# Kernel tuning notes

Measured on AMD Instinct MI355X. Metric: run time of the kernel, lower is better.

Reference implementation:

```python
import jax, jax.numpy as jnp
import numpy as np

N = 100000      # nodes
E = 1000000     # edges
H_DIM = 124     # node embedding dim
CLS_DIM = 4     # node class-logit dim (H_DIM + CLS_DIM = in_features = 128)
POLAR_DIM = 2   # edge_pred_features
HIDDEN = 256
OUT = 2
LN_EPS = 1e-5


def setup_inputs() -> dict:
    key = jax.random.key(0)
    ks = jax.random.split(key, 10)
    in_dim = 2 * (H_DIM + CLS_DIM) + POLAR_DIM  # 258
    return {
        "h": jax.random.normal(ks[0], (N, H_DIM), dtype=jnp.float32),
        "cls": jax.random.normal(ks[1], (N, CLS_DIM), dtype=jnp.float32),
        "polar": jax.random.normal(ks[2], (E, POLAR_DIM), dtype=jnp.float32),
        "src": jax.random.randint(ks[3], (E,), 0, N, dtype=jnp.int64),
        "dst": jax.random.randint(ks[4], (E,), 0, N, dtype=jnp.int64),
        # parameters (PyTorch Linear default-ish init scale)
        "W1": jax.random.normal(ks[5], (in_dim, HIDDEN), dtype=jnp.float32) * (1.0 / np.sqrt(in_dim)),
        "b1": jnp.zeros((HIDDEN,), dtype=jnp.float32),
        "gamma": jnp.ones((HIDDEN,), dtype=jnp.float32),
        "beta": jnp.zeros((HIDDEN,), dtype=jnp.float32),
        "W2": jax.random.normal(ks[6], (HIDDEN, OUT), dtype=jnp.float32) * (1.0 / np.sqrt(HIDDEN)),
        "b2": jnp.zeros((OUT,), dtype=jnp.float32),
    }


def reference(h, cls, polar, src, dst, W1, b1, gamma, beta, W2, b2):
    # softmax over class logits per node (same math as softmax on gathered
    # edge copies, but computed once per node)
    cls_sm = jax.nn.softmax(cls, axis=1)                  # [N, CLS_DIM]
    # gather src/dst node features along edges
    x = jnp.concatenate(
        [h[src], cls_sm[src], polar, h[dst], cls_sm[dst]], axis=1
    )                                                     # [E, 258]
    z = x @ W1 + b1                                        # [E, HIDDEN]
    # LayerNorm
    mu = jnp.mean(z, axis=-1, keepdims=True)
    var = jnp.mean(jnp.square(z - mu), axis=-1, keepdims=True)
    z = (z - mu) * jax.lax.rsqrt(var + LN_EPS) * gamma + beta
    z = jax.nn.relu(z)
    # dropout is identity in eval mode
    score = z @ W2 + b2                                    # [E, OUT]
    return score
```

## Files before the change

### kernel.cpp

```cpp
#include <hip/hip_runtime.h>
#include <hip/hip_bf16.h>

#define NN 100000
#define EE 1000000
#define H_DIM 124
#define PCOLS 512
#define LDK 136
#define CW 132

typedef float f32x4 __attribute__((ext_vector_type(4)));
typedef short bf16x8 __attribute__((ext_vector_type(8)));
typedef _Float16 h2 __attribute__((ext_vector_type(2)));

__device__ __forceinline__ unsigned short f2bf(float f) {
    unsigned int x = __float_as_uint(f);
    unsigned int r = (x + 0x7FFFu + ((x >> 16) & 1u)) >> 16;
    return (unsigned short)r;
}
__device__ __forceinline__ unsigned int pk2bf(float a, float b) {
    return (unsigned int)f2bf(a) | ((unsigned int)f2bf(b) << 16);
}
__device__ __forceinline__ unsigned int pk2h(float a, float b) {
    h2 v = (h2){(_Float16)a, (_Float16)b};
    return __builtin_bit_cast(unsigned int, v);
}

__device__ __forceinline__ float fdot2(h2 a, h2 b, float c) {
#if __has_builtin(__builtin_amdgcn_fdot2)
    return __builtin_amdgcn_fdot2(a, b, c, false);
#else
    return c + (float)a[0] * (float)b[0] + (float)a[1] * (float)b[1];
#endif
}

#if __has_builtin(__builtin_amdgcn_update_dpp)
template <int CTRL>
__device__ __forceinline__ float dpp_add(float x) {
    int xi = __builtin_bit_cast(int, x);
    int t = __builtin_amdgcn_update_dpp(xi, xi, CTRL, 0xF, 0xF, false);
    return x + __builtin_bit_cast(float, t);
}
__device__ __forceinline__ float reduce16(float x) {
    x = dpp_add<0x128>(x);
    x = dpp_add<0x124>(x);
    x = dpp_add<0x122>(x);
    x = dpp_add<0x121>(x);
    return x;
}
#else
__device__ __forceinline__ float reduce16(float x) {
    x += __shfl_xor(x, 8); x += __shfl_xor(x, 4);
    x += __shfl_xor(x, 2); x += __shfl_xor(x, 1);
    return x;
}
#endif

struct alignas(16) H8 { h2 p[4]; };

__global__ __launch_bounds__(256) void build_w1t_ct(const float* __restrict__ W1,
                                                    const float* __restrict__ gamma,
                                                    const float* __restrict__ beta,
                                                    const float* __restrict__ W2,
                                                    unsigned short* __restrict__ W1T,
                                                    uint4* __restrict__ CT) {
    if (blockIdx.x < 256) {
        int t2 = blockIdx.x * 256 + threadIdx.x;
        int j = t2 >> 7, k = t2 & 127;
        int row = (j < 256) ? k : (130 + k);
        int col = (j < 256) ? j : (j - 256);
        W1T[t2] = f2bf(W1[row * 256 + col]);
    } else {
        int t = threadIdx.x;
        if (t < 192) {
            int slot = t % 12, il = t / 12;
            int a = slot >> 1, k = slot & 1;
            int j0 = il * 16 + k * 8;
            float v[8];
            #pragma unroll
            for (int i = 0; i < 8; ++i) {
                int j = j0 + i;
                v[i] = (a == 0) ? W1[128 * 256 + j]
                     : (a == 1) ? W1[129 * 256 + j]
                     : (a == 2) ? gamma[j]
                     : (a == 3) ? beta[j]
                     : (a == 4) ? W2[2 * j]
                     :            W2[2 * j + 1];
            }
            CT[t] = make_uint4(pk2h(v[0], v[1]), pk2h(v[2], v[3]),
                               pk2h(v[4], v[5]), pk2h(v[6], v[7]));
        }
    }
}

__global__ __launch_bounds__(256) void p_gemm(const float* __restrict__ h,
                                              const float* __restrict__ cls,
                                              const unsigned short* __restrict__ W1T,
                                              const float* __restrict__ b1,
                                              _Float16* __restrict__ P) {
    __shared__ alignas(16) unsigned short As[64 * LDK];
    __shared__ alignas(16) unsigned short Bs[128 * LDK];
    float* Cs = (float*)&Bs[0];
    const int m0 = blockIdx.x * 64;
    const int t = threadIdx.x;

    #pragma unroll
    for (int it = 0; it < 4; ++it) {
        int chunk = t + it * 256;
        int r = chunk >> 4, c8 = chunk & 15;
        int row = m0 + r;
        unsigned int w0 = 0, w1 = 0, w2 = 0, w3 = 0;
        if (row < NN) {
            if (c8 < 15) {
                const float* hp = h + (size_t)row * H_DIM + c8 * 8;
                float4 v0 = *(const float4*)(hp);
                float4 v1 = *(const float4*)(hp + 4);
                w0 = pk2bf(v0.x, v0.y); w1 = pk2bf(v0.z, v0.w);
                w2 = pk2bf(v1.x, v1.y); w3 = pk2bf(v1.z, v1.w);
            } else {
                float4 v0 = *(const float4*)(h + (size_t)row * H_DIM + 120);
                float4 c = *(const float4*)(cls + (size_t)row * 4);
                float m = fmaxf(fmaxf(c.x, c.y), fmaxf(c.z, c.w));
                float e0 = __expf(c.x - m), e1 = __expf(c.y - m);
                float e2 = __expf(c.z - m), e3 = __expf(c.w - m);
                float inv = 1.0f / (e0 + e1 + e2 + e3);
                w0 = pk2bf(v0.x, v0.y); w1 = pk2bf(v0.z, v0.w);
                w2 = pk2bf(e0 * inv, e1 * inv); w3 = pk2bf(e2 * inv, e3 * inv);
            }
        }
        *(uint4*)(&As[r * LDK + c8 * 8]) = make_uint4(w0, w1, w2, w3);
    }
    __syncthreads();

    const int wave = t >> 6, lane = t & 63;
    const int wm = wave & 1, wn = wave >> 1;
    const int lm = lane & 15, quad = lane >> 4;

    bf16x8 afrag[4][2];
    #pragma unroll
    for (int s = 0; s < 4; ++s) {
        int k0 = s * 32 + quad * 8;
        #pragma unroll
        for (int mt = 0; mt < 2; ++mt)
            afrag[s][mt] = *(const bf16x8*)(&As[(wm * 32 + mt * 16 + lm) * LDK + k0]);
    }

    for (int cchunk = 0; cchunk < 4; ++cchunk) {
        const int n0 = cchunk * 128;
        if (cchunk) __syncthreads();
        #pragma unroll
        for (int it = 0; it < 8; ++it) {
            int chunk = t + it * 256;
            int r = chunk >> 4, c = chunk & 15;
            float4 v = *(const float4*)(W1T + (n0 + r) * 128 + c * 8);
            *(float4*)(&Bs[r * LDK + c * 8]) = v;
        }
        __syncthreads();

        f32x4 acc[2][4];
        #pragma unroll
        for (int mt = 0; mt < 2; ++mt)
            #pragma unroll
            for (int nt = 0; nt < 4; ++nt)
                acc[mt][nt] = (f32x4){0.f, 0.f, 0.f, 0.f};

        #pragma unroll
        for (int s = 0; s < 4; ++s) {
            int k0 = s * 32 + quad * 8;
            bf16x8 b[4];
            #pragma unroll
            for (int nt = 0; nt < 4; ++nt)
                b[nt] = *(const bf16x8*)(&Bs[(wn * 64 + nt * 16 + lm) * LDK + k0]);
            #pragma unroll
            for (int mt = 0; mt < 2; ++mt)
                #pragma unroll
                for (int nt = 0; nt < 4; ++nt)
                    acc[mt][nt] = __builtin_amdgcn_mfma_f32_16x16x32_bf16(afrag[s][mt], b[nt], acc[mt][nt], 0, 0, 0);
        }
        __syncthreads();

        #pragma unroll
        for (int mt = 0; mt < 2; ++mt)
            #pragma unroll
            for (int nt = 0; nt < 4; ++nt) {
                int col = wn * 64 + nt * 16 + lm;
                int rb  = wm * 32 + mt * 16 + quad * 4;
                #pragma unroll
                for (int r = 0; r < 4; ++r)
                    Cs[(rb + r) * CW + col] = acc[mt][nt][r];
            }
        __syncthreads();

        #pragma unroll
        for (int it = 0; it < 4; ++it) {
            int chunk = t + it * 256;
            int r = chunk >> 4, c8 = chunk & 15;
            float4 a = *(const float4*)(Cs + r * CW + c8 * 8);
            float4 b = *(const float4*)(Cs + r * CW + c8 * 8 + 4);
            if (n0 >= 256) {
                int cb = n0 + c8 * 8 - 256;
                float4 ba = *(const float4*)(b1 + cb);
                float4 bb = *(const float4*)(b1 + cb + 4);
                a.x += ba.x; a.y += ba.y; a.z += ba.z; a.w += ba.w;
                b.x += bb.x; b.y += bb.y; b.z += bb.z; b.w += bb.w;
            }
            uint4 o = make_uint4(pk2h(a.x, a.y), pk2h(a.z, a.w),
                                 pk2h(b.x, b.y), pk2h(b.z, b.w));
            int row = m0 + r;
            if (row < NN)
                *(uint4*)(P + (size_t)row * PCOLS + n0 + c8 * 8) = o;
        }
    }
}

#define K3_BLOCKS 4096
#define K3_WAVES  (K3_BLOCKS * 4)
#define K3_STRIDE (K3_WAVES * 4)
#define K3_ROUNDS 16

__global__ __launch_bounds__(256) void edge_kernel(const _Float16* __restrict__ P,
                                                   const int* __restrict__ src,
                                                   const int* __restrict__ dst,
                                                   const float* __restrict__ polar,
                                                   const uint4* __restrict__ CT,
                                                   const float* __restrict__ b2,
                                                   float* __restrict__ out) {
    const int lane = threadIdx.x & 63;
    const int il   = lane & 15;
    const int g    = lane >> 4;
    const int wid  = blockIdx.x * 4 + (threadIdx.x >> 6);
    const char* Pb = (const char*)P;
    const int e0 = wid * 4 + g;

    uint4 cq[12];
    #pragma unroll
    for (int i = 0; i < 12; ++i) cq[i] = CT[il * 12 + i];
    h2 w0c[8], w1c[8], gc[8], bc[8], w2ac[8], w2bc[8];
    {
        const h2* ch = (const h2*)cq;
        #pragma unroll
        for (int p = 0; p < 8; ++p) {
            w0c[p]  = ch[p];      w1c[p]  = ch[8 + p];
            gc[p]   = ch[16 + p]; bc[p]   = ch[24 + p];
            w2ac[p] = ch[32 + p]; w2bc[p] = ch[40 + p];
        }
    }
    const float b20 = b2[0], b21 = b2[1];
    const h2 zerop = (h2){(_Float16)0.0f, (_Float16)0.0f};

    const unsigned boff_s = (unsigned)(il * 32);
    const unsigned boff_d = (unsigned)(512 + il * 32);

    int   Is[4], Id[4];
    float q[4][2];
    H8 buf[4][4];

    #define LOAD_IDX(slot, r)                                                  \
    {                                                                          \
        int eg = e0 + (r) * K3_STRIDE;                                         \
        int ec = (eg < EE) ? eg : 0;                                           \
        Is[slot] = src[ec]; Id[slot] = dst[ec];                                \
    }
    #define LOAD_Q(slot, r)                                                    \
    {                                                                          \
        int eg = e0 + (r) * K3_STRIDE;                                         \
        int ec = (eg < EE) ? eg : 0;                                           \
        float2 qq = *(const float2*)(polar + 2 * ec);                          \
        q[slot][0] = qq.x; q[slot][1] = qq.y;                                  \
    }
    #define LOAD_P(slot)                                                       \
    {                                                                          \
        unsigned os = (unsigned)Is[slot] * 1024u + boff_s;                     \
        unsigned od = (unsigned)Id[slot] * 1024u + boff_d;                     \
        buf[slot][0] = *(const H8*)(Pb + os);                                  \
        buf[slot][1] = *(const H8*)(Pb + os + 16);                             \
        buf[slot][2] = *(const H8*)(Pb + od);                                  \
        buf[slot][3] = *(const H8*)(Pb + od + 16);                             \
    }

    LOAD_IDX(0, 0) LOAD_IDX(1, 1) LOAD_IDX(2, 2) LOAD_IDX(3, 3)
    LOAD_Q(0, 0) LOAD_Q(1, 1) LOAD_Q(2, 2) LOAD_Q(3, 3)
    LOAD_P(0) LOAD_P(1) LOAD_P(2) LOAD_P(3)
    LOAD_IDX(0, 4) LOAD_IDX(1, 5) LOAD_IDX(2, 6) LOAD_IDX(3, 7)

    #define EDGE_COMPUTE(slot, eg, GUARD)                                      \
    {                                                                          \
        h2 p0 = (h2){(_Float16)q[slot][0], (_Float16)q[slot][0]};              \
        h2 p1 = (h2){(_Float16)q[slot][1], (_Float16)q[slot][1]};              \
        h2 z[8];                                                               \
        float sum = 0.f, ss = 0.f;                                             \
        _Pragma("unroll")                                                      \
        for (int p = 0; p < 8; ++p) {                                          \
            h2 pv = ((p < 4) ? buf[slot][0].p[p] : buf[slot][1].p[p - 4])      \
                  + ((p < 4) ? buf[slot][2].p[p] : buf[slot][3].p[p - 4]);     \
            z[p] = w0c[p] * p0 + (w1c[p] * p1 + pv);                           \
            sum += (float)z[p][0] + (float)z[p][1];                            \
            ss  = fdot2(z[p], z[p], ss);                                       \
        }                                                                      \
        sum = reduce16(sum); ss = reduce16(ss);                                \
        float mu   = sum * (1.0f / 256.0f);                                    \
        float var  = ss * (1.0f / 256.0f) - mu * mu;                           \
        float rstd = rsqrtf(var + 1e-5f);                                      \
        float nmur = -mu * rstd;                                               \
        h2 rsh  = (h2){(_Float16)rstd, (_Float16)rstd};                        \
        h2 nmh  = (h2){(_Float16)nmur, (_Float16)nmur};                        \
        float o0 = 0.f, o1 = 0.f;                                              \
        _Pragma("unroll")                                                      \
        for (int p = 0; p < 8; ++p) {                                          \
            h2 tt = z[p] * rsh + nmh;                                          \
            h2 u = tt * gc[p] + bc[p];                                         \
            u = __builtin_elementwise_max(u, zerop);                           \
            o0 = fdot2(u, w2ac[p], o0);                                        \
            o1 = fdot2(u, w2bc[p], o1);                                        \
        }                                                                      \
        o0 = reduce16(o0); o1 = reduce16(o1);                                  \
        if (il == 0 && (!(GUARD) || (eg) < EE))                                \
            *(float2*)(out + 2 * (eg)) = make_float2(o0 + b20, o1 + b21);      \
    }

    for (int rr = 0; rr < 4; ++rr) {
        int rb = rr * 4;
        #pragma unroll
        for (int u = 0; u < 4; ++u) {
            int eg = e0 + (rb + u) * K3_STRIDE;
            if (rb + u == 15) {
                EDGE_COMPUTE(u, eg, 1)
            } else {
                EDGE_COMPUTE(u, eg, 0)
            }
            LOAD_Q(u, rb + u + 4)
            LOAD_P(u)
            LOAD_IDX(u, rb + u + 8)
        }
    }
    #undef EDGE_COMPUTE
    #undef LOAD_P
    #undef LOAD_Q
    #undef LOAD_IDX
}

extern "C" void kernel_launch(void* const* d_in, const int* in_sizes, int n_in,
                              void* d_out, int out_size, void* d_ws, size_t ws_size,
                              hipStream_t stream) {
    const float* h     = (const float*)d_in[0];
    const float* cls   = (const float*)d_in[1];
    const float* polar = (const float*)d_in[2];
    const int*   src   = (const int*)d_in[3];
    const int*   dst   = (const int*)d_in[4];
    const float* W1    = (const float*)d_in[5];
    const float* b1    = (const float*)d_in[6];
    const float* gamma = (const float*)d_in[7];
    const float* beta  = (const float*)d_in[8];
    const float* W2    = (const float*)d_in[9];
    const float* b2    = (const float*)d_in[10];
    float* out = (float*)d_out;

    char* ws = (char*)d_ws;
    _Float16*       P   = (_Float16*)ws;
    unsigned short* W1T = (unsigned short*)(ws + 102400000);
    uint4*          CT  = (uint4*)(ws + 102531072);

    build_w1t_ct<<<257, 256, 0, stream>>>(W1, gamma, beta, W2, W1T, CT);
    p_gemm<<<1563, 256, 0, stream>>>(h, cls, W1T, b1, P);
    edge_kernel<<<K3_BLOCKS, 256, 0, stream>>>(P, src, dst, polar, CT, b2, out);
}
```

Before: 288.0 us.

## Bucket-sort edges by source node to improve gather locality in edge kernel

Adds a histogram, single-block scan and atomic scatter pass that partially sorts edges by src>>3, writing reordered src/dst/polar/edge-id arrays. The edge kernel then walks contiguous sorted edges per wave and scatters outputs through the stored edge id. The goal is better cache reuse of the per-node P rows in the random src gather. The cost is four extra launches, atomic passes over a million edges, and scattered output writes. It also replaces the fp32 sum of z with a packed fdot2 against ones.

```diff
diff --git a/kernel.cpp b/kernel.cpp
--- a/kernel.cpp
+++ b/kernel.cpp
@@ -7,6 +7,8 @@
 #define PCOLS 512
 #define LDK 136
 #define CW 132
+#define NB 16384
+#define BSH 3
 
 typedef float f32x4 __attribute__((ext_vector_type(4)));
 typedef short bf16x8 __attribute__((ext_vector_type(8)));
@@ -212,24 +214,71 @@
     }
 }
 
+__global__ __launch_bounds__(256) void hist_kernel(const int* __restrict__ src,
+                                                   int* __restrict__ cnt) {
+    int t = blockIdx.x * 256 + threadIdx.x;
+    for (int e = t; e < EE; e += 262144)
+        atomicAdd(&cnt[src[e] >> BSH], 1);
+}
+
+__global__ __launch_bounds__(256) void scan_kernel(const int* __restrict__ cnt,
+                                                   int* __restrict__ off) {
+    __shared__ int part[256];
+    const int t = threadIdx.x;
+    const int base_i = t * (NB / 256);
+    int s = 0;
+    int local[NB / 256];
+    #pragma unroll 8
+    for (int i = 0; i < NB / 256; ++i) { local[i] = cnt[base_i + i]; s += local[i]; }
+    part[t] = s;
+    __syncthreads();
+    for (int d = 1; d < 256; d <<= 1) {
+        int v = (t >= d) ? part[t - d] : 0;
+        __syncthreads();
+        part[t] += v;
+        __syncthreads();
+    }
+    int run = (t == 0) ? 0 : part[t - 1];
+    #pragma unroll 8
+    for (int i = 0; i < NB / 256; ++i) { off[base_i + i] = run; run += local[i]; }
+}
+
+__global__ __launch_bounds__(256) void scatter_kernel(const int* __restrict__ src,
+                                                      const int* __restrict__ dst,
+                                                      const float* __restrict__ polar,
+                                                      int* __restrict__ off,
+                                                      int* __restrict__ srcS,
+                                                      int* __restrict__ dstS,
+                                                      float2* __restrict__ qS,
+                                                      int* __restrict__ eidS) {
+    int t = blockIdx.x * 256 + threadIdx.x;
+    for (int e = t; e < EE; e += 262144) {
+        int s = src[e];
+        int pos = atomicAdd(&off[s >> BSH], 1);
+        srcS[pos] = s;
+        dstS[pos] = dst[e];
+        qS[pos] = *(const float2*)(polar + 2 * e);
+        eidS[pos] = e;
+    }
+}
+
 #define K3_BLOCKS 4096
-#define K3_WAVES  (K3_BLOCKS * 4)
-#define K3_STRIDE (K3_WAVES * 4)
 #define K3_ROUNDS 16
 
 __global__ __launch_bounds__(256) void edge_kernel(const _Float16* __restrict__ P,
-                                                   const int* __restrict__ src,
-                                                   const int* __restrict__ dst,
-                                                   const float* __restrict__ polar,
+                                                   const int* __restrict__ srcS,
+                                                   const int* __restrict__ dstS,
+                                                   const float2* __restrict__ qS,
+                                                   const int* __restrict__ eidS,
                                                    const uint4* __restrict__ CT,
                                                    const float* __restrict__ b2,
                                                    float* __restrict__ out) {
     const int lane = threadIdx.x & 63;
     const int il   = lane & 15;
     const int g    = lane >> 4;
-    const int wid  = blockIdx.x * 4 + (threadIdx.x >> 6);
+    const int wave_id = blockIdx.x * 4 + (threadIdx.x >> 6);
+    const int ebase = wave_id * 64;
     const char* Pb = (const char*)P;
-    const int e0 = wid * 4 + g;
 
     uint4 cq[12];
     #pragma unroll
@@ -245,27 +294,29 @@
         }
     }
     const float b20 = b2[0], b21 = b2[1];
+    const h2 onep  = (h2){(_Float16)1.0f, (_Float16)1.0f};
     const h2 zerop = (h2){(_Float16)0.0f, (_Float16)0.0f};
 
     const unsigned boff_s = (unsigned)(il * 32);
     const unsigned boff_d = (unsigned)(512 + il * 32);
 
-    int   Is[4], Id[4];
+    int   Is[4], Id[4], ei[4];
     float q[4][2];
     H8 buf[4][4];
 
     #define LOAD_IDX(slot, r)                                                  \
     {                                                                          \
-        int eg = e0 + (r) * K3_STRIDE;                                         \
-        int ec = (eg < EE) ? eg : 0;                                           \
-        Is[slot] = src[ec]; Id[slot] = dst[ec];                                \
+        int ec = ebase + (r) * 4 + g;                                          \
+        if (ec >= EE) ec = EE - 1;                                             \
+        Is[slot] = srcS[ec]; Id[slot] = dstS[ec];                              \
     }
     #define LOAD_Q(slot, r)                                                    \
     {                                                                          \
-        int eg = e0 + (r) * K3_STRIDE;                                         \
-        int ec = (eg < EE) ? eg : 0;                                           \
-        float2 qq = *(const float2*)(polar + 2 * ec);                          \
+        int ec = ebase + (r) * 4 + g;                                          \
+        if (ec >= EE) ec = EE - 1;                                             \
+        float2 qq = qS[ec];                                                    \
         q[slot][0] = qq.x; q[slot][1] = qq.y;                                  \
+        ei[slot] = eidS[ec];                                                   \
     }
     #define LOAD_P(slot)                                                       \
     {                                                                          \
@@ -282,7 +333,7 @@
     LOAD_P(0) LOAD_P(1) LOAD_P(2) LOAD_P(3)
     LOAD_IDX(0, 4) LOAD_IDX(1, 5) LOAD_IDX(2, 6) LOAD_IDX(3, 7)
 
-    #define EDGE_COMPUTE(slot, eg, GUARD)                                      \
+    #define EDGE_COMPUTE(slot, eg)                                             \
     {                                                                          \
         h2 p0 = (h2){(_Float16)q[slot][0], (_Float16)q[slot][0]};              \
         h2 p1 = (h2){(_Float16)q[slot][1], (_Float16)q[slot][1]};              \
@@ -293,7 +344,7 @@
             h2 pv = ((p < 4) ? buf[slot][0].p[p] : buf[slot][1].p[p - 4])      \
                   + ((p < 4) ? buf[slot][2].p[p] : buf[slot][3].p[p - 4]);     \
             z[p] = w0c[p] * p0 + (w1c[p] * p1 + pv);                           \
-            sum += (float)z[p][0] + (float)z[p][1];                            \
+            sum = fdot2(z[p], onep, sum);                                      \
             ss  = fdot2(z[p], z[p], ss);                                       \
         }                                                                      \
         sum = reduce16(sum); ss = reduce16(ss);                                \
@@ -313,20 +364,16 @@
             o1 = fdot2(u, w2bc[p], o1);                                        \
         }                                                                      \
         o0 = reduce16(o0); o1 = reduce16(o1);                                  \
-        if (il == 0 && (!(GUARD) || (eg) < EE))                                \
-            *(float2*)(out + 2 * (eg)) = make_float2(o0 + b20, o1 + b21);      \
+        if (il == 0 && (eg) < EE)                                              \
+            *(float2*)(out + 2 * ei[slot]) = make_float2(o0 + b20, o1 + b21);  \
     }
 
     for (int rr = 0; rr < 4; ++rr) {
         int rb = rr * 4;
         #pragma unroll
         for (int u = 0; u < 4; ++u) {
-            int eg = e0 + (rb + u) * K3_STRIDE;
-            if (rb + u == 15) {
-                EDGE_COMPUTE(u, eg, 1)
-            } else {
-                EDGE_COMPUTE(u, eg, 0)
-            }
+            int eg = ebase + (rb + u) * 4 + g;
+            EDGE_COMPUTE(u, eg)
             LOAD_Q(u, rb + u + 4)
             LOAD_P(u)
             LOAD_IDX(u, rb + u + 8)
@@ -355,11 +402,21 @@
     float* out = (float*)d_out;
 
     char* ws = (char*)d_ws;
-    _Float16*       P   = (_Float16*)ws;
-    unsigned short* W1T = (unsigned short*)(ws + 102400000);
-    uint4*          CT  = (uint4*)(ws + 102531072);
+    _Float16*       P    = (_Float16*)ws;
+    unsigned short* W1T  = (unsigned short*)(ws + 102400000);
+    uint4*          CT   = (uint4*)(ws + 102531072);
+    int*            srcS = (int*)(ws + 102535168);
+    int*            dstS = (int*)(ws + 106535168);
+    float2*         qS   = (float2*)(ws + 110535168);
+    int*            eidS = (int*)(ws + 118535168);
+    int*            cnt  = (int*)(ws + 122535168);
+    int*            off  = (int*)(ws + 122600704);
 
     build_w1t_ct<<<257, 256, 0, stream>>>(W1, gamma, beta, W2, W1T, CT);
+    hipMemsetAsync(cnt, 0, NB * 4, stream);
+    hist_kernel<<<1024, 256, 0, stream>>>(src, cnt);
+    scan_kernel<<<1, 256, 0, stream>>>(cnt, off);
+    scatter_kernel<<<1024, 256, 0, stream>>>(src, dst, polar, off, srcS, dstS, qS, eidS);
     p_gemm<<<1563, 256, 0, stream>>>(h, cls, W1T, b1, P);
-    edge_kernel<<<K3_BLOCKS, 256, 0, stream>>>(P, src, dst, polar, CT, b2, out);
-}
+    edge_kernel<<<K3_BLOCKS, 256, 0, stream>>>(P, srcS, dstS, qS, eidS, CT, b2, out);
+}
```

New measurement: 390.1 us. 1.35x slower.
